# Performance work log

Measured on AMD Instinct MI355X. Metric: run time of the kernel, lower is better.

The kernel has to match this reference:

```python
import jax, jax.numpy as jnp
import numpy as np

B_SZ, SEQ, H, P = 4, 8192, 512, 256


def _s5(x, lam_re, lam_im, log_dt, b_re, b_im, c_re, c_im, d):
    """Single-direction S5 diagonal SSM. x: [B,L,H] -> y: [B,L,H]."""
    lam = lam_re + 1j * lam_im                      # [P] complex diagonal A
    dt = jnp.exp(log_dt)                            # [P] ZOH timestep
    a_bar = jnp.exp(lam * dt)                       # [P] discretized A
    b_bar = ((a_bar - 1.0) / lam)[:, None] * (b_re + 1j * b_im)  # [P,H]
    bu = jnp.einsum('blh,ph->blp', x.astype(b_bar.dtype), b_bar)  # [B,L,P]
    a_el = jnp.broadcast_to(a_bar, bu.shape)        # time-invariant A per step

    def comb(e1, e2):  # associative combine for linear recurrence
        a1, s1 = e1
        a2, s2 = e2
        return (a1 * a2, a2 * s1 + s2)

    _, states = jax.lax.associative_scan(comb, (a_el, bu), axis=1)  # [B,L,P]
    c = c_re + 1j * c_im                            # [H,P]
    return jnp.einsum('blp,hp->blh', states, c).real + x * d


def setup_inputs() -> dict:
    key = jax.random.key(0)
    ks = jax.random.split(key, 10)
    return {
        'x': jax.random.normal(ks[0], (B_SZ, SEQ, H), dtype=jnp.float32),
        'Lambda_re': -0.1 - 0.5 * jax.random.uniform(ks[1], (2, P), dtype=jnp.float32),
        'Lambda_im': jnp.pi * jax.random.normal(ks[2], (2, P), dtype=jnp.float32),
        'log_dt': jnp.log(0.001) + (jnp.log(0.1) - jnp.log(0.001)) * jax.random.uniform(ks[3], (2, P), dtype=jnp.float32),
        'B_re': jax.random.normal(ks[4], (2, P, H), dtype=jnp.float32) / np.sqrt(H),
        'B_im': jax.random.normal(ks[5], (2, P, H), dtype=jnp.float32) / np.sqrt(H),
        'C_re': jax.random.normal(ks[6], (2, H, P), dtype=jnp.float32) / np.sqrt(P),
        'C_im': jax.random.normal(ks[7], (2, H, P), dtype=jnp.float32) / np.sqrt(P),
        'D': jax.random.normal(ks[8], (2, H), dtype=jnp.float32),
    }


def reference(x, Lambda_re, Lambda_im, log_dt, B_re, B_im, C_re, C_im, D):
    # fwd(x) + flip(bwd(flip(x)))
    y_f = _s5(x, Lambda_re[0], Lambda_im[0], log_dt[0], B_re[0], B_im[0], C_re[0], C_im[0], D[0])
    x_r = x[:, ::-1]
    y_b = _s5(x_r, Lambda_re[1], Lambda_im[1], log_dt[1], B_re[1], B_im[1], C_re[1], C_im[1], D[1])[:, ::-1]
    return y_f + y_b
```

## Files before the change

kernel.cpp:

```cpp
#include <hip/hip_runtime.h>
#include <math.h>

typedef unsigned short ushort_t;
typedef __bf16 bf16x8 __attribute__((ext_vector_type(8)));
typedef ushort_t ushort8v __attribute__((ext_vector_type(8)));
typedef float f32x4 __attribute__((ext_vector_type(4)));

#define B_SZ   4
#define SEQ    8192
#define M_ROWS (B_SZ * SEQ)
#define CH     128
#define NC     (SEQ / CH)

__device__ __forceinline__ ushort_t f2bf(float f) {
    unsigned u = __float_as_uint(f);
    u = u + 0x7fffu + ((u >> 16) & 1u);
    return (ushort_t)(u >> 16);
}
__device__ __forceinline__ float bf2f(ushort_t b) {
    return __uint_as_float(((unsigned)b) << 16);
}

__device__ __forceinline__ void load16_lds(const void* g, void* l) {
    __builtin_amdgcn_global_load_lds(
        (const __attribute__((address_space(1))) unsigned int*)g,
        (__attribute__((address_space(3))) unsigned int*)l, 16, 0, 0);
}

__global__ void prep_kernel(const float* __restrict__ Lre,
                            const float* __restrict__ Lim,
                            const float* __restrict__ ldt,
                            const float* __restrict__ Bre,
                            const float* __restrict__ Bim,
                            const float* __restrict__ Cre,
                            const float* __restrict__ Cim,
                            float* __restrict__ abar,
                            float* __restrict__ apow,
                            ushort_t* __restrict__ Bmat,
                            ushort_t* __restrict__ Cmat) {
    int idx = blockIdx.x * 256 + threadIdx.x;
    int h = idx & 511;
    int p = (idx >> 9) & 255;
    int d = idx >> 17;
    int ip = d * 256 + p;
    float lr = Lre[ip], li = Lim[ip];
    float dt = expf(ldt[ip]);
    float e   = expf(lr * dt);
    float ang = li * dt;
    float ar = e * cosf(ang), ai = e * sinf(ang);
    float nr = ar - 1.0f, ni = ai;
    float den = lr * lr + li * li;
    float cr = (nr * lr + ni * li) / den;
    float ci = (ni * lr - nr * li) / den;
    float br = Bre[idx], bi = Bim[idx];
    Bmat[(d * 512 + 2 * p) * 512 + h]     = f2bf(cr * br - ci * bi);
    Bmat[(d * 512 + 2 * p + 1) * 512 + h] = f2bf(cr * bi + ci * br);
    if (h == 0) {
        int o = d * 512 + 2 * p;
        abar[o] = ar;  abar[o + 1] = ai;
        float eC = expf(lr * dt * (float)CH);
        float aC = ang * (float)CH;
        apow[o] = eC * cosf(aC);  apow[o + 1] = eC * sinf(aC);
    }
    int p2 = idx & 255;
    int h2 = (idx >> 8) & 511;
    int d2 = idx >> 17;
    Cmat[h2 * 1024 + d2 * 512 + 2 * p2]     = f2bf(Cre[idx]);
    Cmat[h2 * 1024 + d2 * 512 + 2 * p2 + 1] = f2bf(-Cim[idx]);
}

__global__ void conv_x_kernel(const float* __restrict__ x,
                              ushort_t* __restrict__ X16) {
    int i = blockIdx.x * 256 + threadIdx.x;
    float4 v = ((const float4*)x)[i];
    ushort_t o[4] = {f2bf(v.x), f2bf(v.y), f2bf(v.z), f2bf(v.w)};
    *(uint2*)&X16[(size_t)i * 4] = *(const uint2*)o;
}

template<int EPI, int KD_, int NT>
__global__ __launch_bounds__(256)
void gemm_mfma(const ushort_t* __restrict__ A, const ushort_t* __restrict__ Bm,
               ushort_t* __restrict__ Cb, float* __restrict__ Cf,
               const float* __restrict__ X, const float* __restrict__ Dv) {
    __shared__ ushort_t As[128 * 32];
    __shared__ ushort_t Bs[128 * 32];
    const int tid  = threadIdx.x;
    const int lane = tid & 63;
    const int wv   = tid >> 6;
    const int wrow = wv >> 1, wcol = wv & 1;
    const int l15  = lane & 15, lq = lane >> 4;

    const int lin = blockIdx.x;
    const int xcd = lin & 7;
    const int j   = lin >> 3;
    const int mt  = xcd * 32 + j / NT;
    const int nt  = j % NT;
    const int m0 = mt * 128;
    const int n0 = nt * 128;
    const int CN = NT * 128;

    f32x4 acc[4][4];
#pragma unroll
    for (int i = 0; i < 4; ++i)
#pragma unroll
        for (int jj = 0; jj < 4; ++jj)
            acc[i][jj] = (f32x4){0.f, 0.f, 0.f, 0.f};

    const int grow_l = lane >> 2;
    const int gk8    = (lane & 3) * 8;

    const ushort_t* aF = As + (wrow * 64 + l15) * 32 + lq * 8;
    const ushort_t* bF = Bs + (wcol * 64 + l15) * 32 + lq * 8;

    for (int kt = 0; kt < KD_; kt += 32) {
        __syncthreads();
#pragma unroll
        for (int j2 = 0; j2 < 2; ++j2) {
            const int r0 = j2 * 64 + wv * 16;
            load16_lds(&A[(size_t)(m0 + r0 + grow_l) * KD_ + kt + gk8],
                       (void*)&As[r0 * 32]);
            load16_lds(&Bm[(size_t)(n0 + r0 + grow_l) * KD_ + kt + gk8],
                       (void*)&Bs[r0 * 32]);
        }
        __syncthreads();

        bf16x8 af[4], bfr[4];
#pragma unroll
        for (int mi = 0; mi < 4; ++mi) {
            union { ushort8v u; bf16x8 b; } cv;
            cv.u = *(const ushort8v*)(aF + mi * 512);
            af[mi] = cv.b;
        }
#pragma unroll
        for (int ni = 0; ni < 4; ++ni) {
            union { ushort8v u; bf16x8 b; } cv;
            cv.u = *(const ushort8v*)(bF + ni * 512);
            bfr[ni] = cv.b;
        }
#pragma unroll
        for (int mi = 0; mi < 4; ++mi)
#pragma unroll
            for (int ni = 0; ni < 4; ++ni)
                acc[mi][ni] = __builtin_amdgcn_mfma_f32_16x16x32_bf16(
                    af[mi], bfr[ni], acc[mi][ni], 0, 0, 0);
    }

#pragma unroll
    for (int mi = 0; mi < 4; ++mi) {
#pragma unroll
        for (int ni = 0; ni < 4; ++ni) {
            const int col = n0 + wcol * 64 + ni * 16 + l15;
            float dsum = 0.f;
            if (EPI == 1) dsum = Dv[col] + Dv[512 + col];
#pragma unroll
            for (int r = 0; r < 4; ++r) {
                const int row = m0 + wrow * 64 + mi * 16 + lq * 4 + r;
                if (EPI == 0) {
                    Cb[(size_t)row * CN + col] = f2bf(acc[mi][ni][r]);
                } else {
                    const size_t idx = (size_t)row * 512 + col;
                    Cf[idx] = acc[mi][ni][r] + X[idx] * dsum;
                }
            }
        }
    }
}

__global__ __launch_bounds__(512)
void scan_carry(const ushort_t* __restrict__ S, const float* __restrict__ abar,
                float* __restrict__ carry) {
    int b = blockIdx.x, c = blockIdx.y, t = threadIdx.x;
    int dir = t >> 8, p = t & 255;
    float ar = abar[dir * 512 + 2 * p], ai = abar[dir * 512 + 2 * p + 1];
    float sr = 0.f, si = 0.f;
    const ushort_t* base = S + ((size_t)b * SEQ + (size_t)c * CH) * 1024
                             + dir * 512 + 2 * p;
    for (int ii = 0; ii < CH; ++ii) {
        int i = dir ? (CH - 1 - ii) : ii;
        unsigned u = *(const unsigned*)(base + (size_t)i * 1024);
        float re = bf2f((ushort_t)(u & 0xffffu));
        float im = bf2f((ushort_t)(u >> 16));
        float nr = fmaf(ar, sr, fmaf(-ai, si, re));
        float ni = fmaf(ar, si, fmaf(ai, sr, im));
        sr = nr; si = ni;
    }
    int o = (b * NC + c) * 1024 + dir * 512 + 2 * p;
    carry[o] = sr; carry[o + 1] = si;
}

__global__ __launch_bounds__(512)
void scan_comb(const float* __restrict__ carry, float* __restrict__ init,
               const float* __restrict__ apow) {
    int b = blockIdx.x, t = threadIdx.x;
    int dir = t >> 8, p = t & 255;
    float pr = apow[dir * 512 + 2 * p], pi = apow[dir * 512 + 2 * p + 1];
    float sr = 0.f, si = 0.f;
    for (int cc = 0; cc < NC; ++cc) {
        int c = dir ? (NC - 1 - cc) : cc;
        int o = (b * NC + c) * 1024 + dir * 512 + 2 * p;
        init[o] = sr; init[o + 1] = si;
        float cr = carry[o], ci = carry[o + 1];
        float nr = fmaf(pr, sr, fmaf(-pi, si, cr));
        float ni = fmaf(pr, si, fmaf(pi, sr, ci));
        sr = nr; si = ni;
    }
}

__global__ __launch_bounds__(512)
void scan_final(ushort_t* __restrict__ S, const float* __restrict__ abar,
                const float* __restrict__ init) {
    int b = blockIdx.x, c = blockIdx.y, t = threadIdx.x;
    int dir = t >> 8, p = t & 255;
    float ar = abar[dir * 512 + 2 * p], ai = abar[dir * 512 + 2 * p + 1];
    int o = (b * NC + c) * 1024 + dir * 512 + 2 * p;
    float sr = init[o], si = init[o + 1];
    ushort_t* base = S + ((size_t)b * SEQ + (size_t)c * CH) * 1024
                       + dir * 512 + 2 * p;
    for (int ii = 0; ii < CH; ++ii) {
        int i = dir ? (CH - 1 - ii) : ii;
        unsigned* addr = (unsigned*)(base + (size_t)i * 1024);
        unsigned u = *addr;
        float re = bf2f((ushort_t)(u & 0xffffu));
        float im = bf2f((ushort_t)(u >> 16));
        float nr = fmaf(ar, sr, fmaf(-ai, si, re));
        float ni = fmaf(ar, si, fmaf(ai, sr, im));
        sr = nr; si = ni;
        *addr = ((unsigned)f2bf(si) << 16) | (unsigned)f2bf(sr);
    }
}

extern "C" void kernel_launch(void* const* d_in, const int* in_sizes, int n_in,
                              void* d_out, int out_size, void* d_ws, size_t ws_size,
                              hipStream_t stream) {
    const float* x   = (const float*)d_in[0];
    const float* Lre = (const float*)d_in[1];
    const float* Lim = (const float*)d_in[2];
    const float* ldt = (const float*)d_in[3];
    const float* Bre = (const float*)d_in[4];
    const float* Bim = (const float*)d_in[5];
    const float* Cre = (const float*)d_in[6];
    const float* Cim = (const float*)d_in[7];
    const float* Dv  = (const float*)d_in[8];
    float* y = (float*)d_out;
    char* ws = (char*)d_ws;

    ushort_t* SB16 = (ushort_t*)(ws);
    ushort_t* X16  = (ushort_t*)(ws + 67108864);
    ushort_t* Bm16 = (ushort_t*)(ws + 100663296);
    ushort_t* Cm16 = (ushort_t*)(ws + 101711872);
    float* abar  = (float*)(ws + 102760448);
    float* apow  = (float*)(ws + 102764544);
    float* carry = (float*)(ws + 67108864);
    float* initb = (float*)(ws + 68157440);

    prep_kernel<<<1024, 256, 0, stream>>>(Lre, Lim, ldt, Bre, Bim, Cre, Cim,
                                          abar, apow, Bm16, Cm16);
    conv_x_kernel<<<16384, 256, 0, stream>>>(x, X16);

    gemm_mfma<0, 512, 8><<<2048, 256, 0, stream>>>(X16, Bm16, SB16, nullptr,
                                                   nullptr, nullptr);

    dim3 gs(B_SZ, NC);
    scan_carry<<<gs, 512, 0, stream>>>(SB16, abar, carry);
    scan_comb<<<B_SZ, 512, 0, stream>>>(carry, initb, apow);
    scan_final<<<gs, 512, 0, stream>>>(SB16, abar, initb);

    gemm_mfma<1, 1024, 4><<<1024, 256, 0, stream>>>(SB16, Cm16, nullptr, y,
                                                    x, Dv);
}
```

Before: 279.7 us.

## Replace GEMMs with 256x256-tile double-buffered 8-phase pipelined MFMA kernel

Both GEMMs move from a 128x128 tile, 4-wave kernel with sync-load-compute per 32-wide K step to a 256x256 tile, 8-wave kernel. It double-buffers LDS over 64-wide K steps, swizzles the LDS layout to avoid bank conflicts, and interleaves async global-to-LDS loads with MFMA phases using barriers and s_setprio. The intent is to hide memory latency and raise arithmetic intensity per tile. In exchange it uses much more LDS and registers, and the grids shrink to 512 and 256 blocks, which may underfill the GPU's compute units.

Result: faster. 268.6 us (median of 2 runs) (-4.0%).

```diff
diff --git a/kernel.cpp b/kernel.cpp
--- a/kernel.cpp
+++ b/kernel.cpp
@@ -25,6 +25,12 @@
     __builtin_amdgcn_global_load_lds(
         (const __attribute__((address_space(1))) unsigned int*)g,
         (__attribute__((address_space(3))) unsigned int*)l, 16, 0, 0);
+}
+
+__device__ __forceinline__ bf16x8 ldfrag(const ushort_t* p) {
+    union { ushort8v u; bf16x8 b; } cv;
+    cv.u = *(const ushort8v*)p;
+    return cv.b;
 }
 
 __global__ void prep_kernel(const float* __restrict__ Lre,
@@ -78,83 +84,137 @@
 }
 
 template<int EPI, int KD_, int NT>
-__global__ __launch_bounds__(256)
-void gemm_mfma(const ushort_t* __restrict__ A, const ushort_t* __restrict__ Bm,
-               ushort_t* __restrict__ Cb, float* __restrict__ Cf,
-               const float* __restrict__ X, const float* __restrict__ Dv) {
-    __shared__ ushort_t As[128 * 32];
-    __shared__ ushort_t Bs[128 * 32];
+__global__ __launch_bounds__(512, 2)
+void gemm_8ph(const ushort_t* __restrict__ A, const ushort_t* __restrict__ Bm,
+              ushort_t* __restrict__ Cb, float* __restrict__ Cf,
+              const float* __restrict__ X, const float* __restrict__ Dv) {
+    __shared__ ushort_t shA[2][2][256 * 32];
+    __shared__ ushort_t shB[2][2][256 * 32];
+    constexpr int NKT = KD_ / 64;
+
     const int tid  = threadIdx.x;
     const int lane = tid & 63;
     const int wv   = tid >> 6;
-    const int wrow = wv >> 1, wcol = wv & 1;
-    const int l15  = lane & 15, lq = lane >> 4;
+    const int wr = wv >> 2, wc = wv & 3;
+    const int l15 = lane & 15, lq = lane >> 4;
 
     const int lin = blockIdx.x;
     const int xcd = lin & 7;
     const int j   = lin >> 3;
-    const int mt  = xcd * 32 + j / NT;
+    const int mt  = xcd * 16 + j / NT;
     const int nt  = j % NT;
-    const int m0 = mt * 128;
-    const int n0 = nt * 128;
-    const int CN = NT * 128;
-
-    f32x4 acc[4][4];
-#pragma unroll
-    for (int i = 0; i < 4; ++i)
+    const int m0 = mt * 256;
+    const int n0 = nt * 256;
+    const int CN = NT * 256;
+
+    f32x4 acc[8][4];
+#pragma unroll
+    for (int i = 0; i < 8; ++i)
 #pragma unroll
         for (int jj = 0; jj < 4; ++jj)
             acc[i][jj] = (f32x4){0.f, 0.f, 0.f, 0.f};
 
-    const int grow_l = lane >> 2;
-    const int gk8    = (lane & 3) * 8;
-
-    const ushort_t* aF = As + (wrow * 64 + l15) * 32 + lq * 8;
-    const ushort_t* bF = Bs + (wcol * 64 + l15) * 32 + lq * 8;
-
-    for (int kt = 0; kt < KD_; kt += 32) {
-        __syncthreads();
-#pragma unroll
-        for (int j2 = 0; j2 < 2; ++j2) {
-            const int r0 = j2 * 64 + wv * 16;
-            load16_lds(&A[(size_t)(m0 + r0 + grow_l) * KD_ + kt + gk8],
-                       (void*)&As[r0 * 32]);
-            load16_lds(&Bm[(size_t)(n0 + r0 + grow_l) * KD_ + kt + gk8],
-                       (void*)&Bs[r0 * 32]);
-        }
-        __syncthreads();
-
-        bf16x8 af[4], bfr[4];
-#pragma unroll
-        for (int mi = 0; mi < 4; ++mi) {
-            union { ushort8v u; bf16x8 b; } cv;
-            cv.u = *(const ushort8v*)(aF + mi * 512);
-            af[mi] = cv.b;
-        }
+    const int srow = wv * 32 + (lane >> 2);
+    const int sck  = (((lane & 3) ^ ((lane >> 3) & 3))) * 8;
+    const ushort_t* Ag = A  + (size_t)(m0 + srow) * KD_ + sck;
+    const ushort_t* Bg = Bm + (size_t)(n0 + srow) * KD_ + sck;
+
+#define STAGE_A(t, ks) do {                                                   \
+        const ushort_t* g_ = Ag + (size_t)(t) * 64 + (ks) * 32;               \
+        ushort_t* d_ = &shA[(t) & 1][(ks)][wv * 1024];                        \
+        load16_lds(g_, d_);                                                   \
+        load16_lds(g_ + (size_t)16 * KD_, d_ + 512);                          \
+    } while (0)
+#define STAGE_B(t, ks) do {                                                   \
+        const ushort_t* g_ = Bg + (size_t)(t) * 64 + (ks) * 32;               \
+        ushort_t* d_ = &shB[(t) & 1][(ks)][wv * 1024];                        \
+        load16_lds(g_, d_);                                                   \
+        load16_lds(g_ + (size_t)16 * KD_, d_ + 512);                          \
+    } while (0)
+
+    const int rdoff = ((lq ^ ((l15 >> 1) & 3))) * 8;
+    const int rdA = (wr * 128 + l15) * 32 + rdoff;
+    const int rdB = (wc * 64  + l15) * 32 + rdoff;
+
+#define MFMA_PH(bx, by, nlo) do {                                             \
+        __builtin_amdgcn_s_setprio(1);                                        \
+        _Pragma("unroll")                                                     \
+        for (int mi_ = 0; mi_ < 8; ++mi_) {                                   \
+            acc[mi_][nlo]     = __builtin_amdgcn_mfma_f32_16x16x32_bf16(      \
+                af[mi_], bx, acc[mi_][nlo], 0, 0, 0);                         \
+            acc[mi_][nlo + 1] = __builtin_amdgcn_mfma_f32_16x16x32_bf16(      \
+                af[mi_], by, acc[mi_][nlo + 1], 0, 0, 0);                     \
+        }                                                                     \
+        __builtin_amdgcn_s_setprio(0);                                        \
+    } while (0)
+
+    STAGE_A(0, 0); STAGE_A(0, 1); STAGE_B(0, 0); STAGE_B(0, 1);
+    STAGE_A(1, 0); STAGE_B(1, 0); STAGE_A(1, 1);
+    asm volatile("s_waitcnt vmcnt(6)" ::: "memory");
+    __builtin_amdgcn_s_barrier();
+
+    bf16x8 af[8];
+#pragma unroll 2
+    for (int kt = 0; kt < NKT; ++kt) {
+        const int buf = kt & 1;
+        const ushort_t* aS0 = &shA[buf][0][rdA];
+        const ushort_t* aS1 = &shA[buf][1][rdA];
+        const ushort_t* bS0 = &shB[buf][0][rdB];
+        const ushort_t* bS1 = &shB[buf][1][rdB];
+
+        {
+#pragma unroll
+            for (int mi = 0; mi < 8; ++mi) af[mi] = ldfrag(aS0 + mi * 512);
+            bf16x8 b0 = ldfrag(bS0), b1 = ldfrag(bS0 + 512);
+            if (kt + 1 < NKT) STAGE_B(kt + 1, 1);
+            __builtin_amdgcn_s_barrier();
+            MFMA_PH(b0, b1, 0);
+            __builtin_amdgcn_s_barrier();
+        }
+        {
+            bf16x8 b2 = ldfrag(bS0 + 1024), b3 = ldfrag(bS0 + 1536);
+            if (kt + 2 < NKT) STAGE_A(kt + 2, 0);
+            __builtin_amdgcn_s_barrier();
+            MFMA_PH(b2, b3, 2);
+            __builtin_amdgcn_s_barrier();
+        }
+        {
+#pragma unroll
+            for (int mi = 0; mi < 8; ++mi) af[mi] = ldfrag(aS1 + mi * 512);
+            bf16x8 b0 = ldfrag(bS1), b1 = ldfrag(bS1 + 512);
+            if (kt + 2 < NKT) STAGE_B(kt + 2, 0);
+            __builtin_amdgcn_s_barrier();
+            MFMA_PH(b0, b1, 0);
+            __builtin_amdgcn_s_barrier();
+        }
+        {
+            bf16x8 b2 = ldfrag(bS1 + 1024), b3 = ldfrag(bS1 + 1536);
+            if (kt + 2 < NKT) STAGE_A(kt + 2, 1);
+            __builtin_amdgcn_s_barrier();
+            MFMA_PH(b2, b3, 2);
+            if (kt + 1 < NKT) {
+                if (kt + 2 < NKT)
+                    asm volatile("s_waitcnt vmcnt(6)" ::: "memory");
+                else
+                    asm volatile("s_waitcnt vmcnt(0)" ::: "memory");
+                __builtin_amdgcn_s_barrier();
+            }
+        }
+    }
+#undef STAGE_A
+#undef STAGE_B
+#undef MFMA_PH
+
+#pragma unroll
+    for (int mi = 0; mi < 8; ++mi) {
 #pragma unroll
         for (int ni = 0; ni < 4; ++ni) {
-            union { ushort8v u; bf16x8 b; } cv;
-            cv.u = *(const ushort8v*)(bF + ni * 512);
-            bfr[ni] = cv.b;
-        }
-#pragma unroll
-        for (int mi = 0; mi < 4; ++mi)
-#pragma unroll
-            for (int ni = 0; ni < 4; ++ni)
-                acc[mi][ni] = __builtin_amdgcn_mfma_f32_16x16x32_bf16(
-                    af[mi], bfr[ni], acc[mi][ni], 0, 0, 0);
-    }
-
-#pragma unroll
-    for (int mi = 0; mi < 4; ++mi) {
-#pragma unroll
-        for (int ni = 0; ni < 4; ++ni) {
-            const int col = n0 + wcol * 64 + ni * 16 + l15;
+            const int col = n0 + wc * 64 + ni * 16 + l15;
             float dsum = 0.f;
             if (EPI == 1) dsum = Dv[col] + Dv[512 + col];
 #pragma unroll
             for (int r = 0; r < 4; ++r) {
-                const int row = m0 + wrow * 64 + mi * 16 + lq * 4 + r;
+                const int row = m0 + wr * 128 + mi * 16 + lq * 4 + r;
                 if (EPI == 0) {
                     Cb[(size_t)row * CN + col] = f2bf(acc[mi][ni][r]);
                 } else {
@@ -257,14 +317,14 @@
                                           abar, apow, Bm16, Cm16);
     conv_x_kernel<<<16384, 256, 0, stream>>>(x, X16);
 
-    gemm_mfma<0, 512, 8><<<2048, 256, 0, stream>>>(X16, Bm16, SB16, nullptr,
-                                                   nullptr, nullptr);
+    gemm_8ph<0, 512, 4><<<512, 512, 0, stream>>>(X16, Bm16, SB16, nullptr,
+                                                 nullptr, nullptr);
 
     dim3 gs(B_SZ, NC);
     scan_carry<<<gs, 512, 0, stream>>>(SB16, abar, carry);
     scan_comb<<<B_SZ, 512, 0, stream>>>(carry, initb, apow);
     scan_final<<<gs, 512, 0, stream>>>(SB16, abar, initb);
 
-    gemm_mfma<1, 1024, 4><<<1024, 256, 0, stream>>>(SB16, Cm16, nullptr, y,
-                                                    x, Dv);
-}
+    gemm_8ph<1, 1024, 2><<<256, 512, 0, stream>>>(SB16, Cm16, nullptr, y,
+                                                  x, Dv);
+}
```
